# Kernel tuning notes

Measured on AMD Instinct MI355X. Metric: run time of the kernel, lower is better.

## Reference

```python
import jax, jax.numpy as jnp
import numpy as np
from jax import lax

BATCH, T, S, E = 32, 4096, 308, 126  # S ~ 3*nCodons+8 for nCodons=100


def setup_inputs() -> dict:
    key = jax.random.key(0)
    k1, k2, k3, k4 = jax.random.split(key, 4)
    # soft one-hot emission observations [B, T, E] (rows normalized)
    inputs = jax.random.uniform(k1, (BATCH, T, E), dtype=jnp.float32)
    inputs = inputs / inputs.sum(-1, keepdims=True)
    # row-stochastic transition matrix A [S, S]
    A = jax.random.uniform(k2, (S, S), dtype=jnp.float32)
    A = A / A.sum(-1, keepdims=True)
    # row-stochastic emission matrix B [S, E]
    B = jax.random.uniform(k3, (S, E), dtype=jnp.float32)
    B = B / B.sum(-1, keepdims=True)
    # initial state distribution I [S]
    I = jax.random.uniform(k4, (S,), dtype=jnp.float32)
    I = I / I.sum()
    return {"inputs": inputs, "A": A, "B": B, "I": I}


def reference(inputs, A, B, I):
    # Scaled HMM forward algorithm (alpha recursion), loglik accumulated
    # from per-step normalizers, matching CgpHmmCell driven by keras RNN.
    emis = jnp.einsum('bte,se->bts', inputs, B)  # [B, T, S] emission probs

    # t = 0
    alpha0 = I[None, :] * emis[:, 0]             # [B, S]
    z0 = alpha0.sum(-1, keepdims=True)           # [B, 1]
    carry0 = (alpha0 / z0, jnp.log(z0[:, 0]))    # (alpha, loglik [B])

    def step(carry, e_t):
        alpha, ll = carry
        alpha = (alpha @ A) * e_t                # [B, S]
        z = alpha.sum(-1, keepdims=True)
        return (alpha / z, ll + jnp.log(z[:, 0])), None

    emis_rest = jnp.swapaxes(emis[:, 1:], 0, 1)  # [T-1, B, S] for scan
    (alpha_T, loglik), _ = lax.scan(step, carry0, emis_rest)
    # Layer returns loglik_state (per-sequence log-likelihood); the added
    # loss is -mean(loglik), but the forward output is loglik itself.
    return loglik
```

## Files before the change

kernel.cpp:

```cpp
#include <hip/hip_runtime.h>
#include <cstdint>
#include <cstddef>

#define T_LEN 4096
#define S_DIM 308
#define E_DIM 126
#define NBATCH 32
#define CHL 16
#define NCH (T_LEN / CHL)
#define WARM 6
#define NSTEP (CHL + WARM - 1)
#define IW (WARM - 1)
#define QROW 720
#define TC 16
#define ROWB 20480
#define LN128 4.852030263919617f

typedef _Float16 half8 __attribute__((ext_vector_type(8)));
typedef _Float16 half4 __attribute__((ext_vector_type(4)));
typedef float floatx4 __attribute__((ext_vector_type(4)));

union HU8 { uint4 u; half8 h; };
union HU4 { uint2 u; half4 h; };
union HU1 { uint16_t u; _Float16 h; };

__device__ __forceinline__ half8 h8_from_u4(uint4 v) { HU8 t; t.u = v; return t.h; }
__device__ __forceinline__ half4 h4_from_u2(uint2 v) { HU4 t; t.u = v; return t.h; }
__device__ __forceinline__ uint32_t pk2(float x, float y) {
  HU1 a, b; a.h = (_Float16)x; b.h = (_Float16)y;
  return (uint32_t)a.u | ((uint32_t)b.u << 16);
}

__global__ __launch_bounds__(256) void init_pack(const float* __restrict__ A,
                                                 const float* __restrict__ Bm,
                                                 uint32_t* __restrict__ Apk,
                                                 uint32_t* __restrict__ Bfr,
                                                 float* __restrict__ out) {
  int blk = blockIdx.x, tid = threadIdx.x;
  if (blk < 50) {
    int idx = blk * 256 + tid;
    int lane = idx & 63, tile = idx >> 6;
    int kt = tile % 10, nt = tile / 10;
    int n  = nt * 16 + (lane & 15);
    int k0 = kt * 32 + (lane >> 4) * 8;
    uint32_t wv[4];
#pragma unroll
    for (int jj = 0; jj < 4; jj++) {
      int ka = k0 + 2 * jj, kb = ka + 1;
      float x0 = (n < S_DIM && ka < S_DIM) ? A[ka * S_DIM + n] : 0.f;
      float x1 = (n < S_DIM && kb < S_DIM) ? A[kb * S_DIM + n] : 0.f;
      wv[jj] = pk2(x0, x1);
    }
    uint4 o; o.x = wv[0]; o.y = wv[1]; o.z = wv[2]; o.w = wv[3];
    ((uint4*)Apk)[idx] = o;
  } else if (blk < 70) {
    int idx = (blk - 50) * 256 + tid;
    int lane = idx & 63, tile = idx >> 6;
    int kt = tile % 4, nt = tile / 4;
    int n  = nt * 16 + (lane & 15);
    int k0 = kt * 32 + (lane >> 4) * 8;
    uint32_t wv[4];
#pragma unroll
    for (int jj = 0; jj < 4; jj++) {
      int ka = k0 + 2 * jj, kb = ka + 1;
      float x0 = (n < S_DIM && ka < E_DIM) ? 128.f * Bm[n * E_DIM + ka] : 0.f;
      float x1 = (n < S_DIM && kb < E_DIM) ? 128.f * Bm[n * E_DIM + kb] : 0.f;
      wv[jj] = pk2(x0, x1);
    }
    uint4 o; o.x = wv[0]; o.y = wv[1]; o.z = wv[2]; o.w = wv[3];
    ((uint4*)Bfr)[idx] = o;
  } else {
    if (tid < NBATCH) out[tid] = 0.f;
  }
}

__global__ __launch_bounds__(256, 2)
void emis_pack(const uint32_t* __restrict__ Bfr, const float* __restrict__ inp,
               uint2* __restrict__ Efrag) {
  __shared__ __attribute__((aligned(16))) _Float16 inH[2][16 * 136];
  int tc = blockIdx.x, bg = blockIdx.y, bbase = bg * 16;
  int tid = threadIdx.x, lane = tid & 63, w = tid >> 6;
  int gl = lane & 15, quad = lane >> 4;

  half8 bfB[5][4];
#pragma unroll
  for (int q = 0; q < 5; q++)
#pragma unroll
    for (int kt = 0; kt < 4; kt++)
      bfB[q][kt] = h8_from_u4(((const uint4*)Bfr)[((w * 5 + q) * 4 + kt) * 64 + lane]);
#pragma unroll
  for (int q = 0; q < 5; q++)
#pragma unroll
    for (int kt = 0; kt < 4; kt++) asm volatile("" : "+v"(bfB[q][kt]));

  int t0 = tc * TC;
#pragma unroll
  for (int s = 0; s < 4; s++) {
    int flat = tid + s * 256;
    int r = flat >> 6, c2 = flat & 63;
    float2 v; v.x = 0.f; v.y = 0.f;
    if (c2 < 63) v = *(const float2*)(inp + ((size_t)(bbase + r) * T_LEN + t0) * E_DIM + 2 * c2);
    *(uint32_t*)&inH[0][r * 136 + 2 * c2] = pk2(v.x, v.y);
  }
  float2 g[4];
#pragma unroll
  for (int s = 0; s < 4; s++) {
    int flat = tid + s * 256;
    int r = flat >> 6, c2 = flat & 63;
    g[s].x = 0.f; g[s].y = 0.f;
    if (c2 < 63) g[s] = *(const float2*)(inp + ((size_t)(bbase + r) * T_LEN + (t0 + 1)) * E_DIM + 2 * c2);
  }
  __syncthreads();

  for (int i = 0; i < TC; i++) {
    int cur = i & 1, t = t0 + i;
    floatx4 Ea[5];
#pragma unroll
    for (int q = 0; q < 5; q++) Ea[q] = (floatx4){0.f, 0.f, 0.f, 0.f};
#pragma unroll
    for (int kt = 0; kt < 4; kt++) {
      half8 af = h8_from_u4(*(const uint4*)&inH[cur][gl * 136 + kt * 32 + quad * 8]);
#pragma unroll
      for (int q = 0; q < 5; q++)
        Ea[q] = __builtin_amdgcn_mfma_f32_16x16x32_f16(bfB[q][kt], af, Ea[q], 0, 0, 0);
    }
    if (i < TC - 1) {
#pragma unroll
      for (int s = 0; s < 4; s++) {
        int flat = tid + s * 256;
        int r = flat >> 6, c2 = flat & 63;
        uint32_t pv = (c2 < 63) ? pk2(g[s].x, g[s].y) : 0u;
        *(uint32_t*)&inH[cur ^ 1][r * 136 + 2 * c2] = pv;
      }
      int tp = t0 + i + 2; if (tp > T_LEN - 1) tp = T_LEN - 1;
#pragma unroll
      for (int s = 0; s < 4; s++) {
        int flat = tid + s * 256;
        int r = flat >> 6, c2 = flat & 63;
        g[s].x = 0.f; g[s].y = 0.f;
        if (c2 < 63) g[s] = *(const float2*)(inp + ((size_t)(bbase + r) * T_LEN + tp) * E_DIM + 2 * c2);
      }
    }
#pragma unroll
    for (int q = 0; q < 5; q++) {
      uint2 o;
      o.x = pk2(Ea[q][0], Ea[q][1]);
      o.y = pk2(Ea[q][2], Ea[q][3]);
      Efrag[((size_t)t * 40 + bg * 20 + (w * 5 + q)) * 64 + lane] = o;
    }
    __syncthreads();
  }
}

__global__ __launch_bounds__(256, 1)
void hmm_fused5(const uint32_t* __restrict__ Apk, const uint2* __restrict__ Efrag,
                const float* __restrict__ Ivec, float* __restrict__ out) {
  __shared__ __attribute__((aligned(16))) _Float16 QLX[16 * (QROW / 2)];
  __shared__ __attribute__((aligned(16))) _Float16 QLY[16 * (QROW / 2)];
  __shared__ float zX[16], zY[16];
  int bg = blockIdx.y, bbase = bg * 16;
  int cc0 = blockIdx.x * 2, cc1 = cc0 + 1;
  int tid = threadIdx.x, lane = tid & 63, w = tid >> 6;
  int gl = lane & 15, quad = lane >> 4;

  half8 bfA[5][10];
#pragma unroll
  for (int q = 0; q < 5; q++)
#pragma unroll
    for (int kt = 0; kt < 10; kt++)
      bfA[q][kt] = h8_from_u4(((const uint4*)Apk)[((w * 5 + q) * 10 + kt) * 64 + lane]);
#pragma unroll
  for (int q = 0; q < 5; q++)
#pragma unroll
    for (int kt = 0; kt < 10; kt++) asm volatile("" : "+v"(bfA[q][kt]));

  floatx4 PaX[5], PaY[5];
#pragma unroll
  for (int q = 0; q < 5; q++) {
    int sb = (w * 5 + q) * 16 + quad * 4;
#pragma unroll
    for (int r = 0; r < 4; r++) {
      int st = sb + r;
      PaX[q][r] = (st < S_DIM) ? ((cc0 == 0) ? Ivec[st] : 1.0f) : 0.f;
      PaY[q][r] = (st < S_DIM) ? 1.0f : 0.f;
    }
  }
  if (tid < 16) { zX[tid] = 0.f; zY[tid] = 0.f; }

  int tfX = cc0 * CHL - WARM + 1;
  int tfY = cc1 * CHL - WARM + 1;

  ptrdiff_t laneoff = ((ptrdiff_t)bg * 1280 + (ptrdiff_t)(w * 5) * 64 + lane) * 8;
  const char* pX = (const char*)Efrag + (ptrdiff_t)(tfX - 1) * (ptrdiff_t)ROWB + laneoff;
  const char* pY = (const char*)Efrag + (ptrdiff_t)(tfY - 1) * (ptrdiff_t)ROWB + laneoff;

  uint2 EXa[5], EXb[5], EYa[5], EYb[5];
#pragma unroll
  for (int q = 0; q < 5; q++) EXa[q] = *(const uint2*)(pX + q * 512);
  pX += ROWB;
#pragma unroll
  for (int q = 0; q < 5; q++) EXb[q] = *(const uint2*)(pX + q * 512);
  pX += ROWB;
#pragma unroll
  for (int q = 0; q < 5; q++) EYa[q] = *(const uint2*)(pY + q * 512);
  pY += ROWB;
#pragma unroll
  for (int q = 0; q < 5; q++) EYb[q] = *(const uint2*)(pY + q * 512);
  pY += ROWB;

  const int wb = gl * QROW + w * 160 + quad * 8;
  const int rb = gl * QROW + quad * 16;

  float llw0 = 0.f, llw1 = 0.f;

  auto phA = [&](floatx4 (&Pa)[5], uint2 (&E)[5], _Float16* ql, float* zs,
                 bool zchk, bool wr) {
    float qv[5][4];
#pragma unroll
    for (int q = 0; q < 5; q++) {
      half4 ev = h4_from_u2(E[q]);
#pragma unroll
      for (int r = 0; r < 4; r++) qv[q][r] = Pa[q][r] * (float)ev[r];
    }
    if (zchk) {
      float z = 0.f;
#pragma unroll
      for (int q = 0; q < 5; q++) z += (qv[q][0] + qv[q][1]) + (qv[q][2] + qv[q][3]);
      z += __shfl_xor(z, 16); z += __shfl_xor(z, 32);
      if (lane < 16) atomicAdd(&zs[lane], z);
    }
    if (wr) {
#pragma unroll
      for (int q = 0; q < 5; q++) {
        uint2 o; o.x = pk2(qv[q][0], qv[q][1]); o.y = pk2(qv[q][2], qv[q][3]);
        *(uint2*)((char*)ql + wb + q * 32) = o;
      }
    }
  };
  auto phB = [&](floatx4 (&Pa)[5], const _Float16* ql, const char*& p, uint2 (&E)[5]) {
#pragma unroll
    for (int q = 0; q < 5; q++) E[q] = *(const uint2*)(p + q * 512);
    p += ROWB;
#pragma unroll
    for (int q = 0; q < 5; q++) Pa[q] = (floatx4){0.f, 0.f, 0.f, 0.f};
#pragma unroll
    for (int kt = 0; kt < 10; kt++) {
      half8 qf = h8_from_u4(*(const uint4*)((const char*)ql + rb + kt * 64));
#pragma unroll
      for (int q = 0; q < 5; q++)
        Pa[q] = __builtin_amdgcn_mfma_f32_16x16x32_f16(bfA[q][kt], qf, Pa[q], 0, 0, 0);
    }
  };
  auto phBnp = [&](floatx4 (&Pa)[5], const _Float16* ql) {
#pragma unroll
    for (int q = 0; q < 5; q++) Pa[q] = (floatx4){0.f, 0.f, 0.f, 0.f};
#pragma unroll
    for (int kt = 0; kt < 10; kt++) {
      half8 qf = h8_from_u4(*(const uint4*)((const char*)ql + rb + kt * 64));
#pragma unroll
      for (int q = 0; q < 5; q++)
        Pa[q] = __builtin_amdgcn_mfma_f32_16x16x32_f16(bfA[q][kt], qf, Pa[q], 0, 0, 0);
    }
  };

  phA(PaX, EXa, QLX, zX, false, true);
  __syncthreads();

  for (int kk = 0; kk < NSTEP - 1; kk += 2) {
    phB(PaX, QLX, pX, EXa);
    phA(PaY, EYa, QLY, zY, false, true);
    __syncthreads();
    phB(PaY, QLY, pY, EYa);
    phA(PaX, EXb, QLX, zX, (kk + 1 == IW), true);
    __syncthreads();
    if (kk + 1 == IW && tid < 16) { llw0 = cc0 ? logf(zX[tid]) : 0.f; zX[tid] = 0.f; }
    phB(PaX, QLX, pX, EXb);
    if (kk + 1 == IW && cc0 == 0) {
#pragma unroll
      for (int q = 0; q < 5; q++) {
        int sb = (w * 5 + q) * 16 + quad * 4;
#pragma unroll
        for (int r = 0; r < 4; r++) {
          int st = sb + r;
          PaX[q][r] = (st < S_DIM) ? Ivec[st] : 0.f;
        }
      }
    }
    phA(PaY, EYb, QLY, zY, (kk + 1 == IW), true);
    __syncthreads();
    if (kk + 1 == IW && tid < 16) { llw1 = logf(zY[tid]); zY[tid] = 0.f; }
    phB(PaY, QLY, pY, EYb);
    phA(PaX, EXa, QLX, zX, false, true);
    __syncthreads();
  }
  phBnp(PaX, QLX);
  phA(PaY, EYa, QLY, zY, false, true);
  __syncthreads();
  phBnp(PaY, QLY);
  phA(PaX, EXb, QLX, zX, true, false);
  __syncthreads();
  phA(PaY, EYb, QLY, zY, true, false);
  __syncthreads();

  if (tid < 16) {
    float v = (logf(zX[tid]) - llw0) + (logf(zY[tid]) - llw1)
              - 2.0f * (float)CHL * LN128;
    atomicAdd(&out[bbase + tid], v);
  }
}

__global__ __launch_bounds__(640, 3)
void hmm_fused(const uint32_t* __restrict__ Apk,
               const uint32_t* __restrict__ Bfr,
               const float* __restrict__ inp,
               const float* __restrict__ Ivec,
               float* __restrict__ out) {
  __shared__ __attribute__((aligned(16))) _Float16 inH[2][16 * 136];
  __shared__ __attribute__((aligned(16))) _Float16 QLf[2][16 * 336];
  __shared__ float zslot[16];
  int c = blockIdx.x, bbase = blockIdx.y * 16;
  int tid = threadIdx.x, lane = tid & 63, w = tid >> 6;
  int gl = lane & 15, quad = lane >> 4;

  half8 bfA[2][10], bfB[2][4];
#pragma unroll
  for (int q = 0; q < 2; q++) {
#pragma unroll
    for (int kt = 0; kt < 10; kt++)
      bfA[q][kt] = h8_from_u4(((const uint4*)Apk)[((w * 2 + q) * 10 + kt) * 64 + lane]);
#pragma unroll
    for (int kt = 0; kt < 4; kt++)
      bfB[q][kt] = h8_from_u4(((const uint4*)Bfr)[((w * 2 + q) * 4 + kt) * 64 + lane]);
  }
#pragma unroll
  for (int q = 0; q < 2; q++) {
#pragma unroll
    for (int kt = 0; kt < 10; kt++) asm volatile("" : "+v"(bfA[q][kt]));
#pragma unroll
    for (int kt = 0; kt < 4; kt++)  asm volatile("" : "+v"(bfB[q][kt]));
  }

  float Pa[2][4];
#pragma unroll
  for (int q = 0; q < 2; q++) {
    int n = (w * 2 + q) * 16 + gl;
    float v = (n < S_DIM) ? (c == 0 ? Ivec[n] : 1.0f) : 0.f;
#pragma unroll
    for (int r = 0; r < 4; r++) Pa[q][r] = v;
  }
  if (tid < 16) zslot[tid] = 0.f;

  int t_first = (c == 0) ? 1 : (c * CHL - WARM + 1);
  int nstep   = (c == 0) ? (CHL - 1) : (CHL + WARM - 1);
  int iw      = (c == 0) ? -1 : (WARM - 1);
  int t_last  = t_first - 1 + nstep;

  {
    int t0 = t_first - 1;
#pragma unroll
    for (int s = 0; s < 2; s++) {
      int flat = tid + s * 640;
      if (flat < 1024) {
        int r = flat >> 6, c2 = flat & 63;
        float2 v; v.x = 0.f; v.y = 0.f;
        if (c2 < 63) v = *(const float2*)(inp + ((size_t)(bbase + r) * T_LEN + t0) * E_DIM + 2 * c2);
        *(uint32_t*)&inH[0][r * 136 + 2 * c2] = pk2(v.x, v.y);
      }
    }
  }
  float2 g[2];
#pragma unroll
  for (int s = 0; s < 2; s++) {
    int flat = tid + s * 640;
    g[s].x = 0.f; g[s].y = 0.f;
    if (flat < 1024) {
      int r = flat >> 6, c2 = flat & 63;
      if (c2 < 63) g[s] = *(const float2*)(inp + ((size_t)(bbase + r) * T_LEN + t_first) * E_DIM + 2 * c2);
    }
  }
  float llw = 0.f;
  __syncthreads();

  for (int i = 0; i <= nstep; i++) {
    int cur = i & 1, nxt = cur ^ 1;
    floatx4 Ea0 = (floatx4){0.f, 0.f, 0.f, 0.f};
    floatx4 Ea1 = (floatx4){0.f, 0.f, 0.f, 0.f};
#pragma unroll
    for (int kt = 0; kt < 4; kt++) {
      half8 af = h8_from_u4(*(const uint4*)&inH[cur][gl * 136 + kt * 32 + quad * 8]);
      Ea0 = __builtin_amdgcn_mfma_f32_16x16x32_f16(af, bfB[0][kt], Ea0, 0, 0, 0);
      Ea1 = __builtin_amdgcn_mfma_f32_16x16x32_f16(af, bfB[1][kt], Ea1, 0, 0, 0);
    }
    float qv[2][4];
#pragma unroll
    for (int r = 0; r < 4; r++) { qv[0][r] = Pa[0][r] * Ea0[r]; qv[1][r] = Pa[1][r] * Ea1[r]; }
    if (i == iw || i == nstep) {
      float s0 = qv[0][0] + qv[1][0], s1 = qv[0][1] + qv[1][1];
      float s2 = qv[0][2] + qv[1][2], s3 = qv[0][3] + qv[1][3];
#pragma unroll
      for (int off = 1; off <= 8; off <<= 1) {
        s0 += __shfl_xor(s0, off); s1 += __shfl_xor(s1, off);
        s2 += __shfl_xor(s2, off); s3 += __shfl_xor(s3, off);
      }
      if (gl == 0) {
        atomicAdd(&zslot[quad * 4 + 0], s0);
        atomicAdd(&zslot[quad * 4 + 1], s1);
        atomicAdd(&zslot[quad * 4 + 2], s2);
        atomicAdd(&zslot[quad * 4 + 3], s3);
      }
    }
#pragma unroll
    for (int q = 0; q < 2; q++) {
      int k = (w * 2 + q) * 16 + gl;
#pragma unroll
      for (int r = 0; r < 4; r++)
        QLf[cur][(quad * 4 + r) * 336 + k] = (_Float16)qv[q][r];
    }
    if (i < nstep) {
#pragma unroll
      for (int s = 0; s < 2; s++) {
        int flat = tid + s * 640;
        if (flat < 1024) {
          int r = flat >> 6, c2 = flat & 63;
          uint32_t pv = (c2 < 63) ? pk2(g[s].x, g[s].y) : 0u;
          *(uint32_t*)&inH[nxt][r * 136 + 2 * c2] = pv;
        }
      }
    }
    __syncthreads();
    if (i == iw && tid < 16) { llw = logf(zslot[tid]); zslot[tid] = 0.f; }
    if (i == nstep) {
      if (tid < 16) {
        float lle = logf(zslot[tid]);
        atomicAdd(&out[bbase + tid], lle - llw - (float)CHL * LN128);
      }
      break;
    }
    {
      int tp = t_first + i + 1; if (tp > t_last) tp = t_last;
#pragma unroll
      for (int s = 0; s < 2; s++) {
        int flat = tid + s * 640;
        g[s].x = 0.f; g[s].y = 0.f;
        if (flat < 1024) {
          int r = flat >> 6, c2 = flat & 63;
          if (c2 < 63) g[s] = *(const float2*)(inp + ((size_t)(bbase + r) * T_LEN + tp) * E_DIM + 2 * c2);
        }
      }
    }
    floatx4 acc0 = (floatx4){0.f, 0.f, 0.f, 0.f};
    floatx4 acc1 = (floatx4){0.f, 0.f, 0.f, 0.f};
#pragma unroll
    for (int kt = 0; kt < 10; kt++) {
      half8 afv = h8_from_u4(*(const uint4*)&QLf[cur][gl * 336 + kt * 32 + quad * 8]);
      acc0 = __builtin_amdgcn_mfma_f32_16x16x32_f16(afv, bfA[0][kt], acc0, 0, 0, 0);
      acc1 = __builtin_amdgcn_mfma_f32_16x16x32_f16(afv, bfA[1][kt], acc1, 0, 0, 0);
    }
#pragma unroll
    for (int r = 0; r < 4; r++) { Pa[0][r] = acc0[r]; Pa[1][r] = acc1[r]; }
  }
}

extern "C" void kernel_launch(void* const* d_in, const int* in_sizes, int n_in,
                              void* d_out, int out_size, void* d_ws, size_t ws_size,
                              hipStream_t stream) {
  const float* inp = (const float*)d_in[0];
  const float* A   = (const float*)d_in[1];
  const float* Bm  = (const float*)d_in[2];
  const float* Iv  = (const float*)d_in[3];
  float* out = (float*)d_out;

  uint8_t* ws = (uint8_t*)d_ws;
  uint32_t* Apk = (uint32_t*)(ws);
  uint32_t* Bfr = (uint32_t*)(ws + (256u << 10));
  const size_t EOFF   = (size_t)384 << 10;
  const size_t EBYTES = (size_t)T_LEN * ROWB;

  hipLaunchKernelGGL(init_pack, dim3(71), dim3(256), 0, stream, A, Bm, Apk, Bfr, out);
  if (ws_size >= EOFF + EBYTES) {
    uint2* Efrag = (uint2*)(ws + EOFF);
    hipLaunchKernelGGL(emis_pack, dim3(T_LEN / TC, 2), dim3(256), 0, stream, Bfr, inp, Efrag);
    hipLaunchKernelGGL(hmm_fused5, dim3(NCH / 2, NBATCH / 16), dim3(256), 0, stream,
                       Apk, Efrag, Iv, out);
  } else {
    hipLaunchKernelGGL(hmm_fused, dim3(NCH, NBATCH / 16), dim3(640), 0, stream,
                       Apk, Bfr, inp, Iv, out);
  }
}
```

Measured before the change: 160.6 us.

## Split paired-chunk HMM blocks into one chunk per block with swizzled LDS layout

The recurrence kernel now runs one time chunk per 256-thread block instead of interleaving two chunks per block. This doubles the grid and allows two blocks per CU, relying on cross-block occupancy rather than in-block interleaving to hide MFMA and LDS latency. The LDS staging buffer is double-buffered with a swizzled layout, so each lane reads its B fragment with one contiguous 16-byte load. The emission-pack kernel also uses a smaller time tile and a higher occupancy bound. The trade-off is more register pressure under launch_bounds(256,2) and a possible loss of latency hiding if occupancy does not reach two blocks per CU.

After: 327.2 us. +103.7%, slower.

```diff
diff --git a/kernel.cpp b/kernel.cpp
--- a/kernel.cpp
+++ b/kernel.cpp
@@ -11,8 +11,7 @@
 #define WARM 6
 #define NSTEP (CHL + WARM - 1)
 #define IW (WARM - 1)
-#define QROW 720
-#define TC 16
+#define TC 8
 #define ROWB 20480
 #define LN128 4.852030263919617f
 
@@ -74,7 +73,7 @@
   }
 }
 
-__global__ __launch_bounds__(256, 2)
+__global__ __launch_bounds__(256, 4)
 void emis_pack(const uint32_t* __restrict__ Bfr, const float* __restrict__ inp,
                uint2* __restrict__ Efrag) {
   __shared__ __attribute__((aligned(16))) _Float16 inH[2][16 * 136];
@@ -152,14 +151,12 @@
   }
 }
 
-__global__ __launch_bounds__(256, 1)
-void hmm_fused5(const uint32_t* __restrict__ Apk, const uint2* __restrict__ Efrag,
+__global__ __launch_bounds__(256, 2)
+void hmm_fused8(const uint32_t* __restrict__ Apk, const uint2* __restrict__ Efrag,
                 const float* __restrict__ Ivec, float* __restrict__ out) {
-  __shared__ __attribute__((aligned(16))) _Float16 QLX[16 * (QROW / 2)];
-  __shared__ __attribute__((aligned(16))) _Float16 QLY[16 * (QROW / 2)];
-  __shared__ float zX[16], zY[16];
-  int bg = blockIdx.y, bbase = bg * 16;
-  int cc0 = blockIdx.x * 2, cc1 = cc0 + 1;
+  __shared__ __attribute__((aligned(16))) _Float16 QL[2][5120];
+  __shared__ float zsl[16];
+  int c = blockIdx.x, bg = blockIdx.y, bbase = bg * 16;
   int tid = threadIdx.x, lane = tid & 63, w = tid >> 6;
   int gl = lane & 15, quad = lane >> 4;
 
@@ -174,138 +171,89 @@
 #pragma unroll
     for (int kt = 0; kt < 10; kt++) asm volatile("" : "+v"(bfA[q][kt]));
 
-  floatx4 PaX[5], PaY[5];
+  floatx4 Pa[5];
+#pragma unroll
+  for (int q = 0; q < 5; q++)
+#pragma unroll
+    for (int r = 0; r < 4; r++) {
+      int st = (w * 5 + q) * 16 + quad * 4 + r;
+      Pa[q][r] = (st < S_DIM) ? ((c == 0) ? Ivec[st] : 1.0f) : 0.f;
+    }
+  if (tid < 16) zsl[tid] = 0.f;
+
+  int tf = c * CHL - WARM + 1;
+
+  int wboff[5];
 #pragma unroll
   for (int q = 0; q < 5; q++) {
-    int sb = (w * 5 + q) * 16 + quad * 4;
-#pragma unroll
-    for (int r = 0; r < 4; r++) {
-      int st = sb + r;
-      PaX[q][r] = (st < S_DIM) ? ((cc0 == 0) ? Ivec[st] : 1.0f) : 0.f;
-      PaY[q][r] = (st < S_DIM) ? 1.0f : 0.f;
-    }
-  }
-  if (tid < 16) { zX[tid] = 0.f; zY[tid] = 0.f; }
-
-  int tfX = cc0 * CHL - WARM + 1;
-  int tfY = cc1 * CHL - WARM + 1;
-
-  ptrdiff_t laneoff = ((ptrdiff_t)bg * 1280 + (ptrdiff_t)(w * 5) * 64 + lane) * 8;
-  const char* pX = (const char*)Efrag + (ptrdiff_t)(tfX - 1) * (ptrdiff_t)ROWB + laneoff;
-  const char* pY = (const char*)Efrag + (ptrdiff_t)(tfY - 1) * (ptrdiff_t)ROWB + laneoff;
-
-  uint2 EXa[5], EXb[5], EYa[5], EYb[5];
-#pragma unroll
-  for (int q = 0; q < 5; q++) EXa[q] = *(const uint2*)(pX + q * 512);
-  pX += ROWB;
-#pragma unroll
-  for (int q = 0; q < 5; q++) EXb[q] = *(const uint2*)(pX + q * 512);
-  pX += ROWB;
-#pragma unroll
-  for (int q = 0; q < 5; q++) EYa[q] = *(const uint2*)(pY + q * 512);
-  pY += ROWB;
-#pragma unroll
-  for (int q = 0; q < 5; q++) EYb[q] = *(const uint2*)(pY + q * 512);
-  pY += ROWB;
-
-  const int wb = gl * QROW + w * 160 + quad * 8;
-  const int rb = gl * QROW + quad * 16;
-
-  float llw0 = 0.f, llw1 = 0.f;
-
-  auto phA = [&](floatx4 (&Pa)[5], uint2 (&E)[5], _Float16* ql, float* zs,
-                 bool zchk, bool wr) {
-    float qv[5][4];
+    int nt = w * 5 + q;
+    int s0 = nt * 16 + quad * 4;
+    wboff[q] = (s0 >> 5) * 1024 + (((((nt & 1) << 1) | (quad >> 1)) * 16 + gl) << 4)
+             + ((quad & 1) << 3);
+  }
+
+  size_t laneoff = ((size_t)bg * 1280 + (size_t)(w * 5) * 64 + lane) * 8;
+  int r0 = tf - 1; if (r0 < 0) r0 = 0;
+  const char* pE = (const char*)Efrag + (size_t)r0 * ROWB + laneoff;
+  uint2 E[5];
+#pragma unroll
+  for (int q = 0; q < 5; q++) E[q] = *(const uint2*)(pE + q * 512);
+  if (tf - 1 >= 0) pE += ROWB;
+
+  float llw = 0.f;
+
+  for (int ii = 0; ii <= NSTEP; ii++) {
+    int cur = ii & 1;
+    bool zstep = (ii == IW) || (ii == NSTEP);
+    float zacc = 0.f;
 #pragma unroll
     for (int q = 0; q < 5; q++) {
       half4 ev = h4_from_u2(E[q]);
-#pragma unroll
-      for (int r = 0; r < 4; r++) qv[q][r] = Pa[q][r] * (float)ev[r];
-    }
-    if (zchk) {
-      float z = 0.f;
-#pragma unroll
-      for (int q = 0; q < 5; q++) z += (qv[q][0] + qv[q][1]) + (qv[q][2] + qv[q][3]);
-      z += __shfl_xor(z, 16); z += __shfl_xor(z, 32);
-      if (lane < 16) atomicAdd(&zs[lane], z);
-    }
-    if (wr) {
-#pragma unroll
-      for (int q = 0; q < 5; q++) {
-        uint2 o; o.x = pk2(qv[q][0], qv[q][1]); o.y = pk2(qv[q][2], qv[q][3]);
-        *(uint2*)((char*)ql + wb + q * 32) = o;
-      }
-    }
-  };
-  auto phB = [&](floatx4 (&Pa)[5], const _Float16* ql, const char*& p, uint2 (&E)[5]) {
-#pragma unroll
-    for (int q = 0; q < 5; q++) E[q] = *(const uint2*)(p + q * 512);
-    p += ROWB;
-#pragma unroll
-    for (int q = 0; q < 5; q++) Pa[q] = (floatx4){0.f, 0.f, 0.f, 0.f};
+      float v0 = Pa[q][0] * (float)ev[0], v1 = Pa[q][1] * (float)ev[1];
+      float v2 = Pa[q][2] * (float)ev[2], v3 = Pa[q][3] * (float)ev[3];
+      if (zstep) zacc += (v0 + v1) + (v2 + v3);
+      uint2 o; o.x = pk2(v0, v1); o.y = pk2(v2, v3);
+      *(uint2*)((char*)&QL[cur][0] + wboff[q]) = o;
+    }
+    if (zstep) {
+      zacc += __shfl_xor(zacc, 16);
+      zacc += __shfl_xor(zacc, 32);
+      if (lane < 16) atomicAdd(&zsl[lane], zacc);
+    }
+    __syncthreads();
+    if (ii == IW && tid < 16) {
+      llw = c ? logf(zsl[tid]) : 0.f;
+      zsl[tid] = 0.f;
+    }
+    if (ii == NSTEP) {
+      if (tid < 16)
+        atomicAdd(&out[bbase + tid], logf(zsl[tid]) - llw - (float)CHL * LN128);
+      break;
+    }
+#pragma unroll
+    for (int q = 0; q < 5; q++) E[q] = *(const uint2*)(pE + q * 512);
+    if (tf + ii >= 0) pE += ROWB;
+    floatx4 a0 = (floatx4){0.f, 0.f, 0.f, 0.f};
+    floatx4 a1 = a0, a2 = a0, a3 = a0, a4 = a0;
 #pragma unroll
     for (int kt = 0; kt < 10; kt++) {
-      half8 qf = h8_from_u4(*(const uint4*)((const char*)ql + rb + kt * 64));
+      half8 qf = h8_from_u4(*(const uint4*)((const char*)&QL[cur][0] + kt * 1024 + lane * 16));
+      a0 = __builtin_amdgcn_mfma_f32_16x16x32_f16(bfA[0][kt], qf, a0, 0, 0, 0);
+      a1 = __builtin_amdgcn_mfma_f32_16x16x32_f16(bfA[1][kt], qf, a1, 0, 0, 0);
+      a2 = __builtin_amdgcn_mfma_f32_16x16x32_f16(bfA[2][kt], qf, a2, 0, 0, 0);
+      a3 = __builtin_amdgcn_mfma_f32_16x16x32_f16(bfA[3][kt], qf, a3, 0, 0, 0);
+      a4 = __builtin_amdgcn_mfma_f32_16x16x32_f16(bfA[4][kt], qf, a4, 0, 0, 0);
+    }
+    Pa[0] = a0; Pa[1] = a1; Pa[2] = a2; Pa[3] = a3; Pa[4] = a4;
+    if (ii == IW && c == 0) {
 #pragma unroll
       for (int q = 0; q < 5; q++)
-        Pa[q] = __builtin_amdgcn_mfma_f32_16x16x32_f16(bfA[q][kt], qf, Pa[q], 0, 0, 0);
-    }
-  };
-  auto phBnp = [&](floatx4 (&Pa)[5], const _Float16* ql) {
-#pragma unroll
-    for (int q = 0; q < 5; q++) Pa[q] = (floatx4){0.f, 0.f, 0.f, 0.f};
-#pragma unroll
-    for (int kt = 0; kt < 10; kt++) {
-      half8 qf = h8_from_u4(*(const uint4*)((const char*)ql + rb + kt * 64));
-#pragma unroll
-      for (int q = 0; q < 5; q++)
-        Pa[q] = __builtin_amdgcn_mfma_f32_16x16x32_f16(bfA[q][kt], qf, Pa[q], 0, 0, 0);
-    }
-  };
-
-  phA(PaX, EXa, QLX, zX, false, true);
-  __syncthreads();
-
-  for (int kk = 0; kk < NSTEP - 1; kk += 2) {
-    phB(PaX, QLX, pX, EXa);
-    phA(PaY, EYa, QLY, zY, false, true);
-    __syncthreads();
-    phB(PaY, QLY, pY, EYa);
-    phA(PaX, EXb, QLX, zX, (kk + 1 == IW), true);
-    __syncthreads();
-    if (kk + 1 == IW && tid < 16) { llw0 = cc0 ? logf(zX[tid]) : 0.f; zX[tid] = 0.f; }
-    phB(PaX, QLX, pX, EXb);
-    if (kk + 1 == IW && cc0 == 0) {
-#pragma unroll
-      for (int q = 0; q < 5; q++) {
-        int sb = (w * 5 + q) * 16 + quad * 4;
 #pragma unroll
         for (int r = 0; r < 4; r++) {
-          int st = sb + r;
-          PaX[q][r] = (st < S_DIM) ? Ivec[st] : 0.f;
+          int st = (w * 5 + q) * 16 + quad * 4 + r;
+          Pa[q][r] = (st < S_DIM) ? Ivec[st] : 0.f;
         }
-      }
-    }
-    phA(PaY, EYb, QLY, zY, (kk + 1 == IW), true);
-    __syncthreads();
-    if (kk + 1 == IW && tid < 16) { llw1 = logf(zY[tid]); zY[tid] = 0.f; }
-    phB(PaY, QLY, pY, EYb);
-    phA(PaX, EXa, QLX, zX, false, true);
-    __syncthreads();
-  }
-  phBnp(PaX, QLX);
-  phA(PaY, EYa, QLY, zY, false, true);
-  __syncthreads();
-  phBnp(PaY, QLY);
-  phA(PaX, EXb, QLX, zX, true, false);
-  __syncthreads();
-  phA(PaY, EYb, QLY, zY, true, false);
-  __syncthreads();
-
-  if (tid < 16) {
-    float v = (logf(zX[tid]) - llw0) + (logf(zY[tid]) - llw1)
-              - 2.0f * (float)CHL * LN128;
-    atomicAdd(&out[bbase + tid], v);
+    }
   }
 }
 
@@ -480,7 +428,7 @@
   if (ws_size >= EOFF + EBYTES) {
     uint2* Efrag = (uint2*)(ws + EOFF);
     hipLaunchKernelGGL(emis_pack, dim3(T_LEN / TC, 2), dim3(256), 0, stream, Bfr, inp, Efrag);
-    hipLaunchKernelGGL(hmm_fused5, dim3(NCH / 2, NBATCH / 16), dim3(256), 0, stream,
+    hipLaunchKernelGGL(hmm_fused8, dim3(NCH, NBATCH / 16), dim3(256), 0, stream,
                        Apk, Efrag, Iv, out);
   } else {
     hipLaunchKernelGGL(hmm_fused, dim3(NCH, NBATCH / 16), dim3(640), 0, stream,
```
